# Kernel tuning notes

Measured on AMD Instinct MI355X. Metric: run time of the kernel, lower is better.

## Reference

```python
import jax, jax.numpy as jnp
import numpy as np

T = 4096
V = 88   # visible_dim
H = 512  # hidden_dim
R = 512  # rnn_hidden_dim
REG_FACTOR = 0.2
GIBBS_STEPS = 20
EPS = 1e-6


def setup_inputs() -> dict:
    key = jax.random.key(0)
    ks = jax.random.split(key, 8)
    scale = 1.0 / np.sqrt(H)
    return {
        "visible": (jax.random.uniform(ks[0], (T, V)) < 0.5).astype(jnp.float32),
        "rand_h": jax.random.uniform(ks[1], (T - 1, GIBBS_STEPS, H), dtype=jnp.float32),
        "rand_v": jax.random.uniform(ks[2], (T - 1, GIBBS_STEPS, V), dtype=jnp.float32),
        "w": jax.random.normal(ks[3], (H, V), dtype=jnp.float32) * scale,
        "wuu": jax.random.normal(ks[4], (R, R), dtype=jnp.float32) * scale,
        "wuv": jax.random.normal(ks[5], (V, R), dtype=jnp.float32) * scale,
        "wuh": jax.random.normal(ks[6], (H, R), dtype=jnp.float32) * scale,
        "wvu": jax.random.normal(ks[7], (R, V), dtype=jnp.float32) * scale,
        "bv": jnp.zeros((V,), jnp.float32),
        "bh": jnp.zeros((H,), jnp.float32),
        "bu": jnp.zeros((R,), jnp.float32),
        "u0": jnp.zeros((R,), jnp.float32),
    }


def reference(visible, rand_h, rand_v, w, wuu, wuv, wuh, wvu, bv, bh, bu, u0):
    time_steps = visible.shape[0]
    v_seq = visible[1:]  # v_t for t = 1..T-1, shape [T-1, V]

    # RNN state depends only on data, not on Gibbs samples -> single scan.
    def u_step(u_prev, v_t):
        u_new = jnp.tanh(wvu @ v_t + wuu @ u_prev + bu)
        return u_new, u_prev  # emit u_{t-1} (bias conditioning state)

    _, u_prev = jax.lax.scan(u_step, u0, v_seq)  # [T-1, R]

    # Per-timestep RBM biases (F.linear(u, W, b) = u @ W.T + b).
    bh_t = u_prev @ wuh.T + bh  # [T-1, H]
    bv_t = u_prev @ wuv.T + bv  # [T-1, V]

    # 20 Gibbs steps, batched over all time steps at once.
    def gibbs_step(v, rands):
        rh, rv = rands  # [T-1, H], [T-1, V]
        p_h = jax.nn.sigmoid(v @ w.T + bh_t)
        h = jax.nn.relu(jnp.sign(p_h - rh))         # Bernoulli sample
        p_v = jax.nn.sigmoid(h @ w + bv_t)
        v_new = jax.nn.relu(jnp.sign(p_v - rv))
        return v_new, None

    neg, _ = jax.lax.scan(
        gibbs_step, v_seq,
        (jnp.swapaxes(rand_h, 0, 1), jnp.swapaxes(rand_v, 0, 1)),
    )  # negative samples [T-1, V]

    # Cross-entropy between data and sigmoid(bv_t), summed then /time_steps.
    y_t = jax.nn.sigmoid(bv_t)
    total_cost = jnp.sum(
        -v_seq * jnp.log(EPS + y_t) - (1.0 - v_seq) * jnp.log(EPS + 1.0 - y_t)
    ) / time_steps

    reg_term = (jnp.linalg.norm(wuv) + jnp.linalg.norm(wuh)) * REG_FACTOR
    total_cost = total_cost + reg_term

    mse = jnp.mean(jnp.abs(v_seq - neg), axis=1)  # per-timestep, [T-1]
    return total_cost, mse, reg_term
```

## Files before the change

kernel.cpp:

```cpp
#include <hip/hip_runtime.h>
#include <cstdint>
#include <cstddef>

#define T4096 4096
#define TM1 4095
#define NV 88
#define NH 512
#define NR 512
#define GS 20
#define EPSV 1e-6f
#define NCHUNK 512

#define U_OFF 0
#define AB_OFF 2096640
#define SC_OFF 4553640

__device__ __forceinline__ unsigned int agent_load_u32(const unsigned int* p) {
  return __hip_atomic_load(p, __ATOMIC_RELAXED, __HIP_MEMORY_SCOPE_AGENT);
}
__device__ __forceinline__ void agent_store_f32(float* p, float v) {
  __hip_atomic_store(p, v, __ATOMIC_RELAXED, __HIP_MEMORY_SCOPE_AGENT);
}
__device__ __forceinline__ float sigmoidf_(float x) {
  return 1.0f / (1.0f + expf(-x));
}

__device__ __forceinline__ void store_sc0(float* p, float v) {
  asm volatile("global_store_dword %0, %1, off sc0" :: "v"(p), "v"(v) : "memory");
}
__device__ __forceinline__ unsigned load_sc0(const unsigned* p) {
  unsigned r;
  asm volatile("global_load_dword %0, %1, off sc0\n\ts_waitcnt vmcnt(0)"
               : "=v"(r) : "v"(p) : "memory");
  return r;
}
__device__ __forceinline__ void store_sys_f32(float* p, float v) {
  asm volatile("global_store_dword %0, %1, off sc0 sc1" :: "v"(p), "v"(v) : "memory");
}
__device__ __forceinline__ void store_sys_u32(unsigned* p, unsigned v) {
  asm volatile("global_store_dword %0, %1, off sc0 sc1" :: "v"(p), "v"(v) : "memory");
}
__device__ __forceinline__ unsigned load_sys_u32(const unsigned* p) {
  unsigned r;
  asm volatile("global_load_dword %0, %1, off sc0 sc1\n\ts_waitcnt vmcnt(0)"
               : "=v"(r) : "v"(p) : "memory");
  return r;
}
__device__ __forceinline__ void load_sys_f32x4x2(const float* p, float4& a, float4& b) {
  asm volatile("global_load_dwordx4 %0, %2, off sc0 sc1\n\t"
               "global_load_dwordx4 %1, %3, off sc0 sc1\n\t"
               "s_waitcnt vmcnt(0)"
               : "=&v"(a), "=&v"(b)
               : "v"(p), "v"(p + 4) : "memory");
}

__device__ __forceinline__ unsigned poll_nd_sc0(const unsigned* p,
                                                unsigned& s1, unsigned& s2,
                                                unsigned& s3, unsigned& s4) {
  unsigned rA;
  asm volatile(
    "v_mov_b32 %0, -1\n\t"
    "global_load_dword %1, %5, off sc0\n\t"
    "global_load_dword %2, %5, off sc0\n\t"
    "global_load_dword %3, %5, off sc0\n\t"
    "global_load_dword %4, %5, off sc0\n\t"
    "Lr%=:\n\t"
    "s_waitcnt vmcnt(3)\n\t"
    "v_cmp_ne_u32 vcc, -1, %1\n\t"
    "v_cndmask_b32 %0, %0, %1, vcc\n\t"
    "v_cmp_eq_u32 vcc, -1, %0\n\t"
    "s_cbranch_vccz Le%=\n\t"
    "global_load_dword %1, %5, off sc0\n\t"
    "s_waitcnt vmcnt(3)\n\t"
    "v_cmp_ne_u32 vcc, -1, %2\n\t"
    "v_cndmask_b32 %0, %0, %2, vcc\n\t"
    "v_cmp_eq_u32 vcc, -1, %0\n\t"
    "s_cbranch_vccz Le%=\n\t"
    "global_load_dword %2, %5, off sc0\n\t"
    "s_waitcnt vmcnt(3)\n\t"
    "v_cmp_ne_u32 vcc, -1, %3\n\t"
    "v_cndmask_b32 %0, %0, %3, vcc\n\t"
    "v_cmp_eq_u32 vcc, -1, %0\n\t"
    "s_cbranch_vccz Le%=\n\t"
    "global_load_dword %3, %5, off sc0\n\t"
    "s_waitcnt vmcnt(3)\n\t"
    "v_cmp_ne_u32 vcc, -1, %4\n\t"
    "v_cndmask_b32 %0, %0, %4, vcc\n\t"
    "v_cmp_eq_u32 vcc, -1, %0\n\t"
    "s_cbranch_vccz Le%=\n\t"
    "global_load_dword %4, %5, off sc0\n\t"
    "s_branch Lr%=\n\t"
    "Le%=:\n\t"
    : "=&v"(rA), "+v"(s1), "+v"(s2), "+v"(s3), "+v"(s4)
    : "v"(p) : "vcc", "memory");
  return rA;
}
__device__ __forceinline__ unsigned poll_nd_sys(const unsigned* p,
                                                unsigned& s1, unsigned& s2,
                                                unsigned& s3, unsigned& s4) {
  unsigned rA;
  asm volatile(
    "v_mov_b32 %0, -1\n\t"
    "global_load_dword %1, %5, off sc0 sc1\n\t"
    "global_load_dword %2, %5, off sc0 sc1\n\t"
    "global_load_dword %3, %5, off sc0 sc1\n\t"
    "global_load_dword %4, %5, off sc0 sc1\n\t"
    "Lq%=:\n\t"
    "s_waitcnt vmcnt(3)\n\t"
    "v_cmp_ne_u32 vcc, -1, %1\n\t"
    "v_cndmask_b32 %0, %0, %1, vcc\n\t"
    "v_cmp_eq_u32 vcc, -1, %0\n\t"
    "s_cbranch_vccz Lf%=\n\t"
    "global_load_dword %1, %5, off sc0 sc1\n\t"
    "s_waitcnt vmcnt(3)\n\t"
    "v_cmp_ne_u32 vcc, -1, %2\n\t"
    "v_cndmask_b32 %0, %0, %2, vcc\n\t"
    "v_cmp_eq_u32 vcc, -1, %0\n\t"
    "s_cbranch_vccz Lf%=\n\t"
    "global_load_dword %2, %5, off sc0 sc1\n\t"
    "s_waitcnt vmcnt(3)\n\t"
    "v_cmp_ne_u32 vcc, -1, %3\n\t"
    "v_cndmask_b32 %0, %0, %3, vcc\n\t"
    "v_cmp_eq_u32 vcc, -1, %0\n\t"
    "s_cbranch_vccz Lf%=\n\t"
    "global_load_dword %3, %5, off sc0 sc1\n\t"
    "s_waitcnt vmcnt(3)\n\t"
    "v_cmp_ne_u32 vcc, -1, %4\n\t"
    "v_cndmask_b32 %0, %0, %4, vcc\n\t"
    "v_cmp_eq_u32 vcc, -1, %0\n\t"
    "s_cbranch_vccz Lf%=\n\t"
    "global_load_dword %4, %5, off sc0 sc1\n\t"
    "s_branch Lq%=\n\t"
    "Lf%=:\n\t"
    : "=&v"(rA), "+v"(s1), "+v"(s2), "+v"(s3), "+v"(s4)
    : "v"(p) : "vcc", "memory");
  return rA;
}

__global__ __launch_bounds__(256) void k_a(const float* __restrict__ visible,
                                           const float* __restrict__ wvu,
                                           const float* __restrict__ bu,
                                           float* __restrict__ A) {
  __shared__ float vbuf[NV * 8];
  const int tid = threadIdx.x;
  const int t0 = blockIdx.x * 8;
  for (int idx = tid; idx < NV * 8; idx += 256) {
    int j = idx / NV, v = idx - j * NV;
    int t = t0 + j;
    vbuf[v * 8 + j] = (t < TM1) ? visible[(size_t)(t + 1) * NV + v] : 0.f;
  }
  __syncthreads();
  for (int rr = 0; rr < 2; rr++) {
    int r = tid + rr * 256;
    float b0 = bu[r];
    float acc[8];
#pragma unroll
    for (int j = 0; j < 8; j++) acc[j] = b0;
    const float* wr = wvu + (size_t)r * NV;
    for (int v = 0; v < NV; v++) {
      float wv = wr[v];
#pragma unroll
      for (int j = 0; j < 8; j++) acc[j] = fmaf(wv, vbuf[v * 8 + j], acc[j]);
    }
#pragma unroll
    for (int j = 0; j < 8; j++) {
      int t = t0 + j;
      if (t < TM1) A[(size_t)t * NR + r] = acc[j];
    }
  }
}

__global__ __launch_bounds__(256) void k_r(const float* __restrict__ wuv,
                                           const float* __restrict__ wuh,
                                           float* __restrict__ sc) {
  size_t stride = (size_t)gridDim.x * 256;
  size_t gid = (size_t)blockIdx.x * 256 + threadIdx.x;
  float s1 = 0.f, s2 = 0.f;
  for (size_t i = gid; i < (size_t)NV * NR; i += stride) { float x = wuv[i]; s1 = fmaf(x, x, s1); }
  for (size_t i = gid; i < (size_t)NH * NR; i += stride) { float x = wuh[i]; s2 = fmaf(x, x, s2); }
  for (int off = 32; off > 0; off >>= 1) {
    s1 += __shfl_down(s1, off, 64);
    s2 += __shfl_down(s2, off, 64);
  }
  if ((threadIdx.x & 63) == 0) {
    atomicAdd(&sc[1], s1);
    atomicAdd(&sc[2], s2);
  }
}

__global__ __launch_bounds__(512, 2) void k_u13(const float* __restrict__ wuu,
                                                float* A,
                                                const float* __restrict__ u0,
                                                float* __restrict__ U,
                                                unsigned* __restrict__ ub,
                                                const float* __restrict__ visible,
                                                const float* __restrict__ w,
                                                const float* __restrict__ rand_h,
                                                const float* __restrict__ rand_v,
                                                const float* __restrict__ wuh,
                                                const float* __restrict__ wuv,
                                                const float* __restrict__ bh,
                                                const float* __restrict__ bv,
                                                float* __restrict__ out) {
  __shared__ int s_slot;
  __shared__ int s_fast;
  __shared__ int s_cid;
  __shared__ float red2[256];
  __shared__ __align__(16) union {
    struct { float u_buf[NR]; float partials[2][1024]; } p;
    struct { float bht[8 * NH]; float bvt[8 * NV]; float uT[NR * 20]; } b;
    struct { float bht[8 * NH]; float bvt[8 * NV]; float vlds[NV * 10]; float hlds[NH * 20]; } g;
    float occupancy_pad[21000];
  } sh;
  const int tid = threadIdx.x;
  unsigned* claimc = ub + 8;
  unsigned* winner = ub + 16;
  unsigned* hs     = ub + 17;
  unsigned* vd     = ub + 33;
  unsigned* flags  = ub + 64;

  if (tid == 0) {
    unsigned xcd;
    asm volatile("s_getreg_b32 %0, hwreg(HW_REG_XCC_ID, 0, 4)" : "=s"(xcd));
    xcd &= 7u;
    unsigned c = atomicAdd(&claimc[xcd], 1u);
    int slot = -1;
    if (c < 4u) {
      if (c == 3u) atomicCAS(winner, 0xFFFFFFFFu, xcd);
      unsigned wnr;
      do { wnr = agent_load_u32(winner); } while (wnr == 0xFFFFFFFFu);
      if (wnr == xcd) slot = (int)c;
    }
    s_slot = slot;
  }
  __syncthreads();
  const int slot = s_slot;

  if (slot < 0) {
    const int h1 = tid;
    const int tg = tid >> 5, vg = tid & 31;
    const int v0 = vg * 4;
    const bool bact = (vg < 22) && (tg < 8);
    for (;;) {
      if (tid == 0) s_cid = (int)atomicAdd(&ub[56], 1u);
      __syncthreads();
      const int c = s_cid;
      if (c >= NCHUNK) break;
      const int t0c = c * 8;
      const int nt = min(8, TM1 - t0c);
      unsigned need = (unsigned)((t0c + nt - 1 + 31) & ~31);
      if (need > 4064u) need = 4095u;
      if (tid == 0) {
        for (;;) {
          unsigned mn = 0xFFFFFFFFu;
          for (int i = 0; i < 8; i++) { unsigned f = load_sys_u32(&flags[i * 16]); if (f < mn) mn = f; }
          if (mn >= need) break;
          unsigned d = need - mn;
          if (d >= 30u)      __builtin_amdgcn_s_sleep(255);
          else if (d >= 8u)  __builtin_amdgcn_s_sleep(96);
          else               __builtin_amdgcn_s_sleep(16);
        }
      }
      __syncthreads();
      {
        const int tt = tid >> 6, kq = tid & 63;
        const int t = t0c + tt;
        float4 va, vb;
        if (tt < nt) {
          if (t == 0) {
            va = *(const float4*)(u0 + kq * 8);
            vb = *(const float4*)(u0 + kq * 8 + 4);
          } else {
            load_sys_f32x4x2(&A[(size_t)(t - 1) * NR + kq * 8], va, vb);
          }
        } else {
          va.x = va.y = va.z = va.w = 0.f;
          vb.x = vb.y = vb.z = vb.w = 0.f;
        }
        const int k0 = kq * 8;
        sh.b.uT[(k0 + 0) * 20 + tt] = va.x;
        sh.b.uT[(k0 + 1) * 20 + tt] = va.y;
        sh.b.uT[(k0 + 2) * 20 + tt] = va.z;
        sh.b.uT[(k0 + 3) * 20 + tt] = va.w;
        sh.b.uT[(k0 + 4) * 20 + tt] = vb.x;
        sh.b.uT[(k0 + 5) * 20 + tt] = vb.y;
        sh.b.uT[(k0 + 6) * 20 + tt] = vb.z;
        sh.b.uT[(k0 + 7) * 20 + tt] = vb.w;
      }
      __syncthreads();
      float ce = 0.f;
      {
        const int h = tid;
        const bool hasv = tid < NV;
        float acc1[8], accv[8];
#pragma unroll
        for (int i = 0; i < 8; i++) acc1[i] = accv[i] = 0.f;
        const float* w1p = wuh + (size_t)h * NR;
        const float* wvp = wuv + (size_t)(hasv ? tid : 0) * NR;
        for (int k = 0; k < NR; k++) {
          float u8[8];
#pragma unroll
          for (int q = 0; q < 2; q++) *(float4*)(u8 + 4 * q) = *(const float4*)(sh.b.uT + k * 20 + 4 * q);
          float a = w1p[k];
          float cc = hasv ? wvp[k] : 0.f;
#pragma unroll
          for (int i = 0; i < 8; i++) {
            acc1[i] = fmaf(a, u8[i], acc1[i]);
            accv[i] = fmaf(cc, u8[i], accv[i]);
          }
        }
        float bh1 = bh[h];
#pragma unroll
        for (int i = 0; i < 8; i++)
          if (i < nt) sh.b.bht[i * NH + h] = acc1[i] + bh1;
        if (hasv) {
          float bvv = bv[tid];
          for (int i = 0; i < nt; i++) {
            float x = accv[i] + bvv;
            sh.b.bvt[i * NV + tid] = x;
            float y = sigmoidf_(x);
            float vs = visible[(size_t)(t0c + i + 1) * NV + tid];
            ce += -vs * logf(EPSV + y) - (1.f - vs) * logf(EPSV + 1.f - y);
          }
        }
      }
      __syncthreads();
      for (int idx = tid; idx < NV * 8; idx += 512) {
        int j = idx / NV, v = idx - j * NV;
        sh.g.vlds[v * 10 + j] = (j < nt) ? visible[(size_t)(t0c + j + 1) * NV + v] : 0.f;
      }
      __syncthreads();
      for (int k = 0; k < GS; k++) {
        {
          float acc1[8];
#pragma unroll
          for (int i = 0; i < 8; i++) acc1[i] = 0.f;
          const float* w1p = w + (size_t)h1 * NV;
          for (int v = 0; v < NV; v++) {
            float vv[8];
#pragma unroll
            for (int q = 0; q < 2; q++) *(float4*)(vv + 4 * q) = *(const float4*)(sh.g.vlds + v * 10 + 4 * q);
            float a = w1p[v];
#pragma unroll
            for (int i = 0; i < 8; i++) acc1[i] = fmaf(a, vv[i], acc1[i]);
          }
#pragma unroll
          for (int i = 0; i < 8; i++) {
            if (i < nt) {
              size_t t = (size_t)(t0c + i);
              float x1 = acc1[i] + sh.g.bht[i * NH + h1];
              float p1 = sigmoidf_(x1);
              float r1 = rand_h[(t * GS + k) * NH + h1];
              sh.g.hlds[h1 * 20 + i] = (p1 > r1) ? 1.f : 0.f;
            }
          }
        }
        __syncthreads();
        if (bact && tg < nt) {
          float acc[4] = {0.f, 0.f, 0.f, 0.f};
#pragma unroll 4
          for (int h = 0; h < NH; h++) {
            float hv = sh.g.hlds[h * 20 + tg];
            float4 w4 = *(const float4*)(w + (size_t)h * NV + v0);
            acc[0] = fmaf(hv, w4.x, acc[0]);
            acc[1] = fmaf(hv, w4.y, acc[1]);
            acc[2] = fmaf(hv, w4.z, acc[2]);
            acc[3] = fmaf(hv, w4.w, acc[3]);
          }
          size_t t = (size_t)(t0c + tg);
#pragma unroll
          for (int i = 0; i < 4; i++) {
            int v = v0 + i;
            float x = acc[i] + sh.g.bvt[tg * NV + v];
            float p = sigmoidf_(x);
            float r = rand_v[(t * GS + k) * NV + v];
            sh.g.vlds[v * 10 + tg] = (p > r) ? 1.f : 0.f;
          }
        }
        __syncthreads();
      }
      if (tid < nt) {
        float s = 0.f;
        for (int v = 0; v < NV; v++) {
          float vs = visible[(size_t)(t0c + tid + 1) * NV + v];
          s += fabsf(vs - sh.g.vlds[v * 10 + tid]);
        }
        out[1 + t0c + tid] = s / 88.f;
      }
      if (tid < 256) red2[tid] = ce;
      __syncthreads();
      for (int s = 128; s > 0; s >>= 1) {
        if (tid < s) red2[tid] += red2[tid + s];
        __syncthreads();
      }
      if (tid == 0) atomicAdd((float*)ub, red2[0]);
      __syncthreads();
    }
    return;
  }

  if (tid == 0) {
    int fast = 1;
    for (int round = 0; round < 4 && fast; ++round) {
      unsigned* hw = hs + round * 4;
      store_sc0((float*)&hw[slot], 0.0f);
      for (int o = 0; o < 4; ++o) {
        if (o == slot) continue;
        int ok = 0;
        for (int it = 0; it < 300; ++it) {
          if (load_sc0(&hw[o]) != 0xFFFFFFFFu) { ok = 1; break; }
        }
        if (!ok) fast = 0;
      }
    }
    __hip_atomic_store(&vd[slot], (unsigned)(fast ? 1 : 0),
                       __ATOMIC_RELAXED, __HIP_MEMORY_SCOPE_AGENT);
    for (int o = 0; o < 4; ++o) {
      unsigned v;
      do { v = agent_load_u32(&vd[o]); } while (v == 0xFFFFFFFFu);
      if (v != 1u) fast = 0;
    }
    s_fast = fast;
  }
  __syncthreads();
  const int fast = s_fast;

  const int lane = tid & 63;
  const int kc   = tid >> 6;
  const int r0   = slot * 128;
  const bool is_red = (kc >> 1) == slot;
  const int s_row = ((kc & 1) << 6) + lane;
  const int fid = slot * 2 + (kc & 1);
  float* ubw = sh.p.u_buf + kc * 64;

  float WregA[64], WregB[64];
  {
    const float* wra = wuu + (size_t)(r0 + lane) * NR + kc * 64;
    const float* wrb = wuu + (size_t)(r0 + lane + 64) * NR + kc * 64;
#pragma unroll
    for (int i = 0; i < 16; i++) {
      ((float4*)WregA)[i] = ((const float4*)wra)[i];
      ((float4*)WregB)[i] = ((const float4*)wrb)[i];
    }
  }
#pragma unroll
  for (int i = 0; i < 64; i++) asm volatile("" : "+v"(WregA[i]));
#pragma unroll
  for (int i = 0; i < 64; i++) asm volatile("" : "+v"(WregB[i]));

  float val = 0.f, a_cur = 0.f;
  if (is_red) {
    agent_store_f32(&U[r0 + s_row], u0[r0 + s_row]);
    a_cur = A[r0 + s_row];
  }
  unsigned ps1 = 0, ps2 = 0, ps3 = 0, ps4 = 0;
  __syncthreads();

#define KU_STEP(T_, UVAL_) do {                                                \
    ubw[lane] = (UVAL_);                                                       \
    float acc0 = 0.f, acc1 = 0.f;                                              \
    _Pragma("unroll")                                                          \
    for (int i = 0; i < 64; i += 4) {                                          \
      float4 uv = *(const float4*)(ubw + i);                                   \
      acc0 = fmaf(WregA[i],     uv.x, acc0);                                   \
      acc1 = fmaf(WregB[i],     uv.x, acc1);                                   \
      acc0 = fmaf(WregA[i + 1], uv.y, acc0);                                   \
      acc1 = fmaf(WregB[i + 1], uv.y, acc1);                                   \
      acc0 = fmaf(WregA[i + 2], uv.z, acc0);                                   \
      acc1 = fmaf(WregB[i + 2], uv.z, acc1);                                   \
      acc0 = fmaf(WregA[i + 3], uv.w, acc0);                                   \
      acc1 = fmaf(WregB[i + 3], uv.w, acc1);                                   \
    }                                                                          \
    float* pb = sh.p.partials[(T_) & 1];                                       \
    pb[kc * 128 + lane] = acc0;                                                \
    pb[kc * 128 + lane + 64] = acc1;                                           \
    __syncthreads();                                                           \
    if (is_red) {                                                              \
      float s = a_cur;                                                         \
      _Pragma("unroll")                                                        \
      for (int kk = 0; kk < 8; kk++) s += pb[kk * 128 + s_row];                \
      val = tanhf(s);                                                          \
      if (fast) store_sc0(&U[(size_t)(T_) * NR + r0 + s_row], val);            \
      else      agent_store_f32(&U[(size_t)(T_) * NR + r0 + s_row], val);      \
      store_sys_f32(&A[(size_t)((T_) - 1) * NR + r0 + s_row], val);            \
      a_cur = A[(size_t)(T_) * NR + r0 + s_row];    \
      if (((T_) & 31) == 0) {                                                  \
        asm volatile("s_waitcnt vmcnt(0)" ::: "memory");                       \
        if (lane == 0) store_sys_u32(&flags[fid * 16], (unsigned)(T_));        \
      }                                                                        \
    }                                                                          \
  } while (0)

  KU_STEP(1, u0[kc * 64 + lane]);
  for (int t = 2; t <= TM1 - 1; t++) {
    float u_val;
    if (is_red) {
      u_val = val;
    } else {
      const unsigned* p = (const unsigned*)(U + (size_t)(t - 1) * NR) + kc * 64 + lane;
      unsigned wv = fast ? poll_nd_sc0(p, ps1, ps2, ps3, ps4)
                         : poll_nd_sys(p, ps1, ps2, ps3, ps4);
      u_val = __uint_as_float(wv);
    }
    KU_STEP(t, u_val);
  }
#undef KU_STEP
  if (is_red) {
    asm volatile("s_waitcnt vmcnt(0)" ::: "memory");
    if (lane == 0) store_sys_u32(&flags[fid * 16], 4095u);
  }
}

__global__ void k_f(const float* __restrict__ sc, float* __restrict__ out) {
  float reg = 0.2f * (sqrtf(sc[1]) + sqrtf(sc[2]));
  out[0] = sc[0] / 4096.f + reg;
  out[4096] = reg;
}

extern "C" void kernel_launch(void* const* d_in, const int* in_sizes, int n_in,
                              void* d_out, int out_size, void* d_ws, size_t ws_size,
                              hipStream_t stream) {
  const float* visible = (const float*)d_in[0];
  const float* rand_h  = (const float*)d_in[1];
  const float* rand_v  = (const float*)d_in[2];
  const float* w       = (const float*)d_in[3];
  const float* wuu     = (const float*)d_in[4];
  const float* wuv     = (const float*)d_in[5];
  const float* wuh     = (const float*)d_in[6];
  const float* wvu     = (const float*)d_in[7];
  const float* bv      = (const float*)d_in[8];
  const float* bh      = (const float*)d_in[9];
  const float* bu      = (const float*)d_in[10];
  const float* u0      = (const float*)d_in[11];
  float* out = (float*)d_out;
  float* ws = (float*)d_ws;

  float* Uarr = ws + U_OFF;
  float* Aarr = ws + AB_OFF;
  float* sc   = ws + SC_OFF;
  unsigned* ub = (unsigned*)sc;

  hipMemsetAsync(Uarr, 0xFF, (size_t)TM1 * NR * sizeof(float), stream);
  hipMemsetAsync(sc, 0, 64, stream);
  hipMemsetAsync((char*)sc + 64, 0xFF, 96, stream);
  hipMemsetAsync((char*)sc + 160, 0, 608, stream);

  k_a<<<512, 256, 0, stream>>>(visible, wvu, bu, Aarr);
  k_r<<<64, 256, 0, stream>>>(wuv, wuh, sc);
  k_u13<<<256, 512, 0, stream>>>(wuu, Aarr, u0, Uarr, ub,
                                 visible, w, rand_h, rand_v,
                                 wuh, wuv, bh, bv, out);
  k_f<<<1, 1, 0, stream>>>(sc, out);
}
```

Before: 5.169 ms.

## Offload u-state publishing and progress flags to a dedicated fifth relay workgroup

A fifth workgroup on the winning XCD now polls each new recurrent state row in U and copies it into A with system-scope stores, then posts the progress flags every 32 steps. The recurrence workgroups no longer do the system-scope A store, the vmcnt drain or the flag store on their serial critical path. In exchange it adds an extra polling hop, so consumer workgroups see published state later and one more workgroup spins on memory.

New measurement: 5.316 ms. +2.8%, slower.

```diff
diff --git a/kernel.cpp b/kernel.cpp
--- a/kernel.cpp
+++ b/kernel.cpp
@@ -33,9 +33,6 @@
   asm volatile("global_load_dword %0, %1, off sc0\n\ts_waitcnt vmcnt(0)"
                : "=v"(r) : "v"(p) : "memory");
   return r;
-}
-__device__ __forceinline__ void store_sys_f32(float* p, float v) {
-  asm volatile("global_store_dword %0, %1, off sc0 sc1" :: "v"(p), "v"(v) : "memory");
 }
 __device__ __forceinline__ void store_sys_u32(unsigned* p, unsigned v) {
   asm volatile("global_store_dword %0, %1, off sc0 sc1" :: "v"(p), "v"(v) : "memory");
@@ -137,6 +134,89 @@
   return rA;
 }
 
+__device__ __forceinline__ unsigned poll_rd_sc0(const unsigned* p) {
+  unsigned rA, r0, r1, r2, r3;
+  asm volatile(
+    "s_waitcnt vmcnt(0)\n\t"
+    "v_mov_b32 %0, -1\n\t"
+    "global_load_dword %1, %5, off sc0\n\t"
+    "global_load_dword %2, %5, off sc0\n\t"
+    "global_load_dword %3, %5, off sc0\n\t"
+    "global_load_dword %4, %5, off sc0\n\t"
+    "Lr%=:\n\t"
+    "s_waitcnt vmcnt(3)\n\t"
+    "v_cmp_ne_u32 vcc, -1, %1\n\t"
+    "v_cndmask_b32 %0, %0, %1, vcc\n\t"
+    "v_cmp_eq_u32 vcc, -1, %0\n\t"
+    "s_cbranch_vccz Le%=\n\t"
+    "global_load_dword %1, %5, off sc0\n\t"
+    "s_waitcnt vmcnt(3)\n\t"
+    "v_cmp_ne_u32 vcc, -1, %2\n\t"
+    "v_cndmask_b32 %0, %0, %2, vcc\n\t"
+    "v_cmp_eq_u32 vcc, -1, %0\n\t"
+    "s_cbranch_vccz Le%=\n\t"
+    "global_load_dword %2, %5, off sc0\n\t"
+    "s_waitcnt vmcnt(3)\n\t"
+    "v_cmp_ne_u32 vcc, -1, %3\n\t"
+    "v_cndmask_b32 %0, %0, %3, vcc\n\t"
+    "v_cmp_eq_u32 vcc, -1, %0\n\t"
+    "s_cbranch_vccz Le%=\n\t"
+    "global_load_dword %3, %5, off sc0\n\t"
+    "s_waitcnt vmcnt(3)\n\t"
+    "v_cmp_ne_u32 vcc, -1, %4\n\t"
+    "v_cndmask_b32 %0, %0, %4, vcc\n\t"
+    "v_cmp_eq_u32 vcc, -1, %0\n\t"
+    "s_cbranch_vccz Le%=\n\t"
+    "global_load_dword %4, %5, off sc0\n\t"
+    "s_branch Lr%=\n\t"
+    "Le%=:\n\t"
+    "s_waitcnt vmcnt(0)\n\t"
+    : "=&v"(rA), "=&v"(r0), "=&v"(r1), "=&v"(r2), "=&v"(r3)
+    : "v"(p) : "vcc", "memory");
+  return rA;
+}
+__device__ __forceinline__ unsigned poll_rd_sys(const unsigned* p) {
+  unsigned rA, r0, r1, r2, r3;
+  asm volatile(
+    "s_waitcnt vmcnt(0)\n\t"
+    "v_mov_b32 %0, -1\n\t"
+    "global_load_dword %1, %5, off sc0 sc1\n\t"
+    "global_load_dword %2, %5, off sc0 sc1\n\t"
+    "global_load_dword %3, %5, off sc0 sc1\n\t"
+    "global_load_dword %4, %5, off sc0 sc1\n\t"
+    "Lq%=:\n\t"
+    "s_waitcnt vmcnt(3)\n\t"
+    "v_cmp_ne_u32 vcc, -1, %1\n\t"
+    "v_cndmask_b32 %0, %0, %1, vcc\n\t"
+    "v_cmp_eq_u32 vcc, -1, %0\n\t"
+    "s_cbranch_vccz Lf%=\n\t"
+    "global_load_dword %1, %5, off sc0 sc1\n\t"
+    "s_waitcnt vmcnt(3)\n\t"
+    "v_cmp_ne_u32 vcc, -1, %2\n\t"
+    "v_cndmask_b32 %0, %0, %2, vcc\n\t"
+    "v_cmp_eq_u32 vcc, -1, %0\n\t"
+    "s_cbranch_vccz Lf%=\n\t"
+    "global_load_dword %2, %5, off sc0 sc1\n\t"
+    "s_waitcnt vmcnt(3)\n\t"
+    "v_cmp_ne_u32 vcc, -1, %3\n\t"
+    "v_cndmask_b32 %0, %0, %3, vcc\n\t"
+    "v_cmp_eq_u32 vcc, -1, %0\n\t"
+    "s_cbranch_vccz Lf%=\n\t"
+    "global_load_dword %3, %5, off sc0 sc1\n\t"
+    "s_waitcnt vmcnt(3)\n\t"
+    "v_cmp_ne_u32 vcc, -1, %4\n\t"
+    "v_cndmask_b32 %0, %0, %4, vcc\n\t"
+    "v_cmp_eq_u32 vcc, -1, %0\n\t"
+    "s_cbranch_vccz Lf%=\n\t"
+    "global_load_dword %4, %5, off sc0 sc1\n\t"
+    "s_branch Lq%=\n\t"
+    "Lf%=:\n\t"
+    "s_waitcnt vmcnt(0)\n\t"
+    : "=&v"(rA), "=&v"(r0), "=&v"(r1), "=&v"(r2), "=&v"(r3)
+    : "v"(p) : "vcc", "memory");
+  return rA;
+}
+
 __global__ __launch_bounds__(256) void k_a(const float* __restrict__ visible,
                                            const float* __restrict__ wvu,
                                            const float* __restrict__ bu,
@@ -188,7 +268,7 @@
   }
 }
 
-__global__ __launch_bounds__(512, 2) void k_u13(const float* __restrict__ wuu,
+__global__ __launch_bounds__(512, 2) void k_u14(const float* __restrict__ wuu,
                                                 float* A,
                                                 const float* __restrict__ u0,
                                                 float* __restrict__ U,
@@ -225,7 +305,7 @@
     xcd &= 7u;
     unsigned c = atomicAdd(&claimc[xcd], 1u);
     int slot = -1;
-    if (c < 4u) {
+    if (c < 5u) {
       if (c == 3u) atomicCAS(winner, 0xFFFFFFFFu, xcd);
       unsigned wnr;
       do { wnr = agent_load_u32(winner); } while (wnr == 0xFFFFFFFFu);
@@ -235,6 +315,36 @@
   }
   __syncthreads();
   const int slot = s_slot;
+
+  if (slot == 4) {
+    if (tid == 0) {
+      int fast = 1;
+      for (int o = 0; o < 4; ++o) {
+        unsigned v;
+        do { v = agent_load_u32(&vd[o]); } while (v == 0xFFFFFFFFu);
+        if (v != 1u) fast = 0;
+      }
+      s_fast = fast;
+    }
+    __syncthreads();
+    const int fast = s_fast;
+    const int lane = tid & 63;
+    const int kc   = tid >> 6;
+    unsigned* aw = (unsigned*)A + kc * 64 + lane;
+    const unsigned* up = (const unsigned*)U + kc * 64 + lane;
+    for (int t = 1; t <= TM1 - 1; t++) {
+      const unsigned* p = up + (size_t)t * NR;
+      unsigned wv = fast ? poll_rd_sc0(p) : poll_rd_sys(p);
+      store_sys_u32(aw + (size_t)(t - 1) * NR, wv);
+      if ((t & 31) == 0) {
+        asm volatile("s_waitcnt vmcnt(0)" ::: "memory");
+        if (lane == 0) store_sys_u32(&flags[kc * 16], (unsigned)t);
+      }
+    }
+    asm volatile("s_waitcnt vmcnt(0)" ::: "memory");
+    if (lane == 0) store_sys_u32(&flags[kc * 16], 4095u);
+    return;
+  }
 
   if (slot < 0) {
     const int h1 = tid;
@@ -430,7 +540,6 @@
   const int r0   = slot * 128;
   const bool is_red = (kc >> 1) == slot;
   const int s_row = ((kc & 1) << 6) + lane;
-  const int fid = slot * 2 + (kc & 1);
   float* ubw = sh.p.u_buf + kc * 64;
 
   float WregA[64], WregB[64];
@@ -482,12 +591,7 @@
       val = tanhf(s);                                                          \
       if (fast) store_sc0(&U[(size_t)(T_) * NR + r0 + s_row], val);            \
       else      agent_store_f32(&U[(size_t)(T_) * NR + r0 + s_row], val);      \
-      store_sys_f32(&A[(size_t)((T_) - 1) * NR + r0 + s_row], val);            \
       a_cur = A[(size_t)(T_) * NR + r0 + s_row];    \
-      if (((T_) & 31) == 0) {                                                  \
-        asm volatile("s_waitcnt vmcnt(0)" ::: "memory");                       \
-        if (lane == 0) store_sys_u32(&flags[fid * 16], (unsigned)(T_));        \
-      }                                                                        \
     }                                                                          \
   } while (0)
 
@@ -505,10 +609,6 @@
     KU_STEP(t, u_val);
   }
 #undef KU_STEP
-  if (is_red) {
-    asm volatile("s_waitcnt vmcnt(0)" ::: "memory");
-    if (lane == 0) store_sys_u32(&flags[fid * 16], 4095u);
-  }
 }
 
 __global__ void k_f(const float* __restrict__ sc, float* __restrict__ out) {
@@ -547,7 +647,7 @@
 
   k_a<<<512, 256, 0, stream>>>(visible, wvu, bu, Aarr);
   k_r<<<64, 256, 0, stream>>>(wuv, wuh, sc);
-  k_u13<<<256, 512, 0, stream>>>(wuu, Aarr, u0, Uarr, ub,
+  k_u14<<<256, 512, 0, stream>>>(wuu, Aarr, u0, Uarr, ub,
                                  visible, w, rand_h, rand_v,
                                  wuh, wuv, bh, bv, out);
   k_f<<<1, 1, 0, stream>>>(sc, out);
```
